# Performance work log

Measured on AMD Instinct MI355X. Metric: run time of the kernel, lower is better.

## Reference

```python
import jax, jax.numpy as jnp
import numpy as np

H = 1024      # hidden_size
E = 8         # num_experts
I = 4 * H     # intermediate_size
B, S = 2, 2048


def setup_inputs() -> dict:
    key = jax.random.key(0)
    ks = jax.random.split(key, 7)
    s_h = 1.0 / np.sqrt(H)
    s_i = 1.0 / np.sqrt(I)
    return {
        "x": jax.random.normal(ks[0], (B, S, H), dtype=jnp.float32),
        "gate_w": jax.random.uniform(ks[1], (H, E), jnp.float32, -s_h, s_h),
        "gate_b": jax.random.uniform(ks[2], (E,), jnp.float32, -s_h, s_h),
        "W1": jax.random.uniform(ks[3], (E, H, I), jnp.float32, -s_h, s_h),
        "b1": jax.random.uniform(ks[4], (E, I), jnp.float32, -s_h, s_h),
        "W2": jax.random.uniform(ks[5], (E, I, H), jnp.float32, -s_i, s_i),
        "b2": jax.random.uniform(ks[6], (E, H), jnp.float32, -s_i, s_i),
    }


def reference(x, gate_w, gate_b, W1, b1, W2, b2):
    b, s, h = x.shape
    flat = x.reshape(-1, h)                      # [T, H]
    T = flat.shape[0]
    e = gate_b.shape[0]

    # Router: softmax -> top-2 -> renormalize
    logits = flat @ gate_w + gate_b              # [T, E]
    probs = jax.nn.softmax(logits, axis=-1)
    top_w, top_idx = jax.lax.top_k(probs, 2)     # [T, 2]
    top_w = top_w / (top_w.sum(axis=-1, keepdims=True) + 1e-6)

    # Dense per-token gate weight matrix [T, E] (0 except top-2 slots)
    gate_full = jnp.zeros((T, e), flat.dtype).at[
        jnp.arange(T)[:, None], top_idx
    ].add(top_w)

    # All experts on all tokens (dense, math-equivalent combine via gate_full)
    hmid = jax.nn.gelu(jnp.einsum('th,ehi->eti', flat, W1) + b1[:, None, :],
                       approximate=True)         # [E, T, I]
    y = jnp.einsum('eti,eih->eth', hmid, W2) + b2[:, None, :]  # [E, T, H]
    out = jnp.einsum('te,eth->th', gate_full, y)  # weighted combine
    return out.reshape(b, s, h)
```

## Files before the change

### kernel.cpp

```cpp
#include <hip/hip_runtime.h>
#include <hip/hip_bf16.h>
#include <math.h>

#define H_DIM 1024
#define E_NUM 8
#define I_DIM 4096
#define T_NUM 4096
#define CAP   8192

typedef __attribute__((ext_vector_type(8))) short bf16x8;
typedef __attribute__((ext_vector_type(4))) float f32x4;

typedef const __attribute__((address_space(1))) void* gptr_t;
typedef __attribute__((address_space(3))) void* lptr_t;

__device__ inline unsigned short f2bf(float f) {
  union { __hip_bfloat16 h; unsigned short u; } cv;
  cv.h = __float2bfloat16(f);
  return cv.u;
}

__global__ void router_kernel(const float* __restrict__ x,
                              const float* __restrict__ gw,
                              const float* __restrict__ gb,
                              int* __restrict__ cnt,
                              int* __restrict__ list,
                              float* __restrict__ tokw) {
  const int t = blockIdx.x;
  const int l = threadIdx.x;
  const float* xr = x + (size_t)t * H_DIM;
  float acc[E_NUM];
#pragma unroll
  for (int e = 0; e < E_NUM; ++e) acc[e] = 0.f;
#pragma unroll
  for (int j = 0; j < H_DIM / 64; ++j) {
    const int h = l + j * 64;
    const float xv = xr[h];
    const float4* g = (const float4*)(gw + (size_t)h * E_NUM);
    const float4 g0 = g[0], g1 = g[1];
    acc[0] += xv * g0.x; acc[1] += xv * g0.y; acc[2] += xv * g0.z; acc[3] += xv * g0.w;
    acc[4] += xv * g1.x; acc[5] += xv * g1.y; acc[6] += xv * g1.z; acc[7] += xv * g1.w;
  }
#pragma unroll
  for (int off = 32; off > 0; off >>= 1) {
#pragma unroll
    for (int e = 0; e < E_NUM; ++e) acc[e] += __shfl_down(acc[e], off, 64);
  }
  if (l == 0) {
    float lg[E_NUM], mx = -1e30f;
#pragma unroll
    for (int e = 0; e < E_NUM; ++e) { lg[e] = acc[e] + gb[e]; mx = fmaxf(mx, lg[e]); }
    float p[E_NUM], s = 0.f;
#pragma unroll
    for (int e = 0; e < E_NUM; ++e) { p[e] = expf(lg[e] - mx); s += p[e]; }
    const float inv = 1.f / s;
#pragma unroll
    for (int e = 0; e < E_NUM; ++e) p[e] *= inv;
    int i0 = 0;
#pragma unroll
    for (int e = 1; e < E_NUM; ++e) if (p[e] > p[i0]) i0 = e;
    int i1 = (i0 == 0) ? 1 : 0;
#pragma unroll
    for (int e = 0; e < E_NUM; ++e) if (e != i0 && p[e] > p[i1]) i1 = e;
    const float denom = p[i0] + p[i1] + 1e-6f;
    const float w0 = p[i0] / denom, w1 = p[i1] / denom;
    int pos = atomicAdd(&cnt[i0], 1);
    list[i0 * CAP + pos] = t * 2;
    tokw[t * 2] = w0;
    pos = atomicAdd(&cnt[i1], 1);
    list[i1 * CAP + pos] = t * 2 + 1;
    tokw[t * 2 + 1] = w1;
  }
}

__global__ void scan_kernel(const int* __restrict__ cnt, int* __restrict__ base) {
  if (threadIdx.x == 0 && blockIdx.x == 0) {
    int b = 0;
    for (int e = 0; e < E_NUM; ++e) { base[e] = b; b += cnt[e]; }
  }
}

__launch_bounds__(256)
__global__ void cvt_x_kernel(const float* __restrict__ x, unsigned short* __restrict__ xb) {
  const size_t i = ((size_t)blockIdx.x * 256 + threadIdx.x) * 8;
  const float4 v0 = *(const float4*)(x + i);
  const float4 v1 = *(const float4*)(x + i + 4);
  unsigned short t[8];
  t[0] = f2bf(v0.x); t[1] = f2bf(v0.y); t[2] = f2bf(v0.z); t[3] = f2bf(v0.w);
  t[4] = f2bf(v1.x); t[5] = f2bf(v1.y); t[6] = f2bf(v1.z); t[7] = f2bf(v1.w);
  *(f32x4*)(xb + i) = *(const f32x4*)t;
}

__launch_bounds__(256)
__global__ void transpose_cvt_kernel(const float* __restrict__ src,
                                     unsigned short* __restrict__ dst,
                                     int R, int C) {
  const int e = blockIdx.z;
  const int r0 = blockIdx.y * 32;
  const int c0 = blockIdx.x * 128;
  const float* s = src + (size_t)e * R * C;
  unsigned short* d = dst + (size_t)e * R * C;
  __shared__ unsigned short Lt[32 * 130];
  const int tid = threadIdx.x;
#pragma unroll
  for (int m = 0; m < 4; ++m) {
    const int li = tid + m * 256;
    const int r = li >> 5;
    const int cg = (li & 31) * 4;
    const float4 v = *(const float4*)(s + (size_t)(r0 + r) * C + c0 + cg);
    Lt[r * 130 + cg + 0] = f2bf(v.x);
    Lt[r * 130 + cg + 1] = f2bf(v.y);
    Lt[r * 130 + cg + 2] = f2bf(v.z);
    Lt[r * 130 + cg + 3] = f2bf(v.w);
  }
  __syncthreads();
#pragma unroll
  for (int m = 0; m < 2; ++m) {
    const int li = tid + m * 256;
    const int col = li >> 2;
    const int rg = (li & 3) * 8;
    unsigned short tmp[8];
#pragma unroll
    for (int j = 0; j < 8; ++j) tmp[j] = Lt[(rg + j) * 130 + col];
    *(f32x4*)(d + (size_t)(c0 + col) * R + r0 + rg) = *(const f32x4*)tmp;
  }
}

__launch_bounds__(256)
__global__ void gemm1_pre_kernel(const unsigned short* __restrict__ xb,
                                 const unsigned short* __restrict__ W1t,
                                 const float* __restrict__ b1,
                                 const int* __restrict__ cnt,
                                 const int* __restrict__ base,
                                 const int* __restrict__ list,
                                 unsigned short* __restrict__ hmid) {
  const int e = blockIdx.z;
  const int c = cnt[e];
  const int m0 = blockIdx.y * 128;
  if (m0 >= c) return;
  const int n0 = blockIdx.x * 128;

  __shared__ int toks[128];
  __shared__ __align__(16) unsigned short As[128 * 32];
  __shared__ __align__(16) unsigned short Bs[128 * 32];

  const int tid = threadIdx.x;
  if (tid < 128) {
    int idx = m0 + tid; if (idx >= c) idx = c - 1;
    toks[tid] = list[e * CAP + idx] >> 1;
  }
  __syncthreads();

  const int lane = tid & 63;
  const int wave = tid >> 6;
  const int wm = (wave >> 1) * 64;
  const int wn = (wave & 1) * 64;
  const int l16 = lane & 15;
  const int quad = lane >> 4;

  const int rA0 = tid >> 2;
  const int rA1 = rA0 + 64;
  const int kg0 = (tid & 3) * 8;
  const unsigned short* W1e = W1t + (size_t)e * H_DIM * I_DIM;

  const unsigned short* aSrc0 = xb + (size_t)toks[rA0] * H_DIM + kg0;
  const unsigned short* aSrc1 = xb + (size_t)toks[rA1] * H_DIM + kg0;
  const unsigned short* bSrc0 = W1e + (size_t)(n0 + rA0) * H_DIM + kg0;
  const unsigned short* bSrc1 = W1e + (size_t)(n0 + rA1) * H_DIM + kg0;
  char* aDst0 = (char*)As + wave * 1024;
  char* aDst1 = (char*)As + 4096 + wave * 1024;
  char* bDst0 = (char*)Bs + wave * 1024;
  char* bDst1 = (char*)Bs + 4096 + wave * 1024;

  f32x4 acc[16];
#pragma unroll
  for (int i = 0; i < 16; ++i) acc[i] = (f32x4){0.f, 0.f, 0.f, 0.f};

  for (int k0 = 0; k0 < H_DIM; k0 += 32) {
    __builtin_amdgcn_global_load_lds((gptr_t)(aSrc0 + k0), (lptr_t)aDst0, 16, 0, 0);
    __builtin_amdgcn_global_load_lds((gptr_t)(aSrc1 + k0), (lptr_t)aDst1, 16, 0, 0);
    __builtin_amdgcn_global_load_lds((gptr_t)(bSrc0 + k0), (lptr_t)bDst0, 16, 0, 0);
    __builtin_amdgcn_global_load_lds((gptr_t)(bSrc1 + k0), (lptr_t)bDst1, 16, 0, 0);
    __syncthreads();
    bf16x8 a[4], b[4];
#pragma unroll
    for (int mf = 0; mf < 4; ++mf)
      a[mf] = *(const bf16x8*)&As[(wm + mf * 16 + l16) * 32 + quad * 8];
#pragma unroll
    for (int nf = 0; nf < 4; ++nf)
      b[nf] = *(const bf16x8*)&Bs[(wn + nf * 16 + l16) * 32 + quad * 8];
#pragma unroll
    for (int mf = 0; mf < 4; ++mf)
#pragma unroll
      for (int nf = 0; nf < 4; ++nf)
        acc[mf * 4 + nf] = __builtin_amdgcn_mfma_f32_16x16x32_bf16(
            a[mf], b[nf], acc[mf * 4 + nf], 0, 0, 0);
    __syncthreads();
  }

  const int hb = base[e];
#pragma unroll
  for (int mf = 0; mf < 4; ++mf) {
#pragma unroll
    for (int reg = 0; reg < 4; ++reg) {
      const int row = wm + mf * 16 + quad * 4 + reg;
      const int gr = m0 + row;
      if (gr < c) {
#pragma unroll
        for (int nf = 0; nf < 4; ++nf) {
          const int col = n0 + wn + nf * 16 + l16;
          const float v = acc[mf * 4 + nf][reg] + b1[e * I_DIM + col];
          const float u = v + 0.044715f * v * v * v;
          const float g = v / (1.f + __expf(-1.5957691216057308f * u));
          hmid[(size_t)(hb + gr) * I_DIM + col] = f2bf(g);
        }
      }
    }
  }
}

__launch_bounds__(256)
__global__ void gemm2_pre_kernel(const unsigned short* __restrict__ hmid,
                                 const unsigned short* __restrict__ W2t,
                                 const float* __restrict__ b2,
                                 const int* __restrict__ cnt,
                                 const int* __restrict__ base,
                                 const int* __restrict__ list,
                                 const float* __restrict__ tokw,
                                 float* __restrict__ out) {
  const int e = blockIdx.z;
  const int c = cnt[e];
  const int m0 = blockIdx.y * 128;
  if (m0 >= c) return;
  const int n0 = blockIdx.x * 128;

  __shared__ int ents[128];
  __shared__ int arow[128];
  __shared__ __align__(16) unsigned short As[128 * 32];
  __shared__ __align__(16) unsigned short Bs[128 * 32];

  const int tid = threadIdx.x;
  const int hb = base[e];
  if (tid < 128) {
    int idx = m0 + tid; if (idx >= c) idx = c - 1;
    ents[tid] = list[e * CAP + idx];
    arow[tid] = hb + idx;
  }
  __syncthreads();

  const int lane = tid & 63;
  const int wave = tid >> 6;
  const int wm = (wave >> 1) * 64;
  const int wn = (wave & 1) * 64;
  const int l16 = lane & 15;
  const int quad = lane >> 4;

  const int rA0 = tid >> 2;
  const int rA1 = rA0 + 64;
  const int kg0 = (tid & 3) * 8;
  const unsigned short* W2e = W2t + (size_t)e * I_DIM * H_DIM;

  const unsigned short* aSrc0 = hmid + (size_t)arow[rA0] * I_DIM + kg0;
  const unsigned short* aSrc1 = hmid + (size_t)arow[rA1] * I_DIM + kg0;
  const unsigned short* bSrc0 = W2e + (size_t)(n0 + rA0) * I_DIM + kg0;
  const unsigned short* bSrc1 = W2e + (size_t)(n0 + rA1) * I_DIM + kg0;
  char* aDst0 = (char*)As + wave * 1024;
  char* aDst1 = (char*)As + 4096 + wave * 1024;
  char* bDst0 = (char*)Bs + wave * 1024;
  char* bDst1 = (char*)Bs + 4096 + wave * 1024;

  f32x4 acc[16];
#pragma unroll
  for (int i = 0; i < 16; ++i) acc[i] = (f32x4){0.f, 0.f, 0.f, 0.f};

  for (int k0 = 0; k0 < I_DIM; k0 += 32) {
    __builtin_amdgcn_global_load_lds((gptr_t)(aSrc0 + k0), (lptr_t)aDst0, 16, 0, 0);
    __builtin_amdgcn_global_load_lds((gptr_t)(aSrc1 + k0), (lptr_t)aDst1, 16, 0, 0);
    __builtin_amdgcn_global_load_lds((gptr_t)(bSrc0 + k0), (lptr_t)bDst0, 16, 0, 0);
    __builtin_amdgcn_global_load_lds((gptr_t)(bSrc1 + k0), (lptr_t)bDst1, 16, 0, 0);
    __syncthreads();
    bf16x8 a[4], b[4];
#pragma unroll
    for (int mf = 0; mf < 4; ++mf)
      a[mf] = *(const bf16x8*)&As[(wm + mf * 16 + l16) * 32 + quad * 8];
#pragma unroll
    for (int nf = 0; nf < 4; ++nf)
      b[nf] = *(const bf16x8*)&Bs[(wn + nf * 16 + l16) * 32 + quad * 8];
#pragma unroll
    for (int mf = 0; mf < 4; ++mf)
#pragma unroll
      for (int nf = 0; nf < 4; ++nf)
        acc[mf * 4 + nf] = __builtin_amdgcn_mfma_f32_16x16x32_bf16(
            a[mf], b[nf], acc[mf * 4 + nf], 0, 0, 0);
    __syncthreads();
  }

#pragma unroll
  for (int mf = 0; mf < 4; ++mf) {
#pragma unroll
    for (int reg = 0; reg < 4; ++reg) {
      const int row = wm + mf * 16 + quad * 4 + reg;
      const int gr = m0 + row;
      if (gr < c) {
        const int ent = ents[row];
        const int t = ent >> 1;
        const float wgt = tokw[ent];
#pragma unroll
        for (int nf = 0; nf < 4; ++nf) {
          const int col = n0 + wn + nf * 16 + l16;
          const float v = acc[mf * 4 + nf][reg] + b2[e * H_DIM + col];
          atomicAdd(&out[(size_t)t * H_DIM + col], wgt * v);
        }
      }
    }
  }
}

__launch_bounds__(256)
__global__ void gemm1_fb_kernel(const float* __restrict__ x,
                                const float* __restrict__ W1,
                                const float* __restrict__ b1,
                                const int* __restrict__ cnt,
                                const int* __restrict__ base,
                                const int* __restrict__ list,
                                unsigned short* __restrict__ hmid) {
  const int e = blockIdx.z;
  const int c = cnt[e];
  const int m0 = blockIdx.y * 128;
  if (m0 >= c) return;
  const int n0 = blockIdx.x * 128;
  __shared__ int toks[128];
  __shared__ __align__(16) unsigned short As[128 * 40];
  __shared__ __align__(16) unsigned short Bs[128 * 40];
  const int tid = threadIdx.x;
  if (tid < 128) {
    int idx = m0 + tid; if (idx >= c) idx = c - 1;
    toks[tid] = list[e * CAP + idx] >> 1;
  }
  __syncthreads();
  const int lane = tid & 63, wave = tid >> 6;
  const int wm = (wave >> 1) * 64, wn = (wave & 1) * 64;
  const int l16 = lane & 15, quad = lane >> 4;
  f32x4 acc[16];
#pragma unroll
  for (int i = 0; i < 16; ++i) acc[i] = (f32x4){0.f, 0.f, 0.f, 0.f};
  const float* W1e = W1 + (size_t)e * H_DIM * I_DIM;
  for (int kt = 0; kt < H_DIM / 32; ++kt) {
    const int k0 = kt * 32;
#pragma unroll
    for (int i = 0; i < 2; ++i) {
      const int idx = tid + i * 256;
      const int row = idx >> 2, g = idx & 3;
      const float* src = x + (size_t)toks[row] * H_DIM + k0 + g * 8;
      const float4 v0 = *(const float4*)(src);
      const float4 v1 = *(const float4*)(src + 4);
      unsigned short tmp[8];
      tmp[0] = f2bf(v0.x); tmp[1] = f2bf(v0.y); tmp[2] = f2bf(v0.z); tmp[3] = f2bf(v0.w);
      tmp[4] = f2bf(v1.x); tmp[5] = f2bf(v1.y); tmp[6] = f2bf(v1.z); tmp[7] = f2bf(v1.w);
      *(f32x4*)&As[row * 40 + g * 8] = *(const f32x4*)tmp;
    }
#pragma unroll
    for (int i = 0; i < 2; ++i) {
      const int idx = tid + i * 256;
      const int n = idx & 127, g = idx >> 7;
      const float* src = W1e + (size_t)(k0 + g * 8) * I_DIM + n0 + n;
      unsigned short tmp[8];
#pragma unroll
      for (int kk = 0; kk < 8; ++kk) tmp[kk] = f2bf(src[(size_t)kk * I_DIM]);
      *(f32x4*)&Bs[n * 40 + g * 8] = *(const f32x4*)tmp;
    }
    __syncthreads();
    bf16x8 a[4], b[4];
#pragma unroll
    for (int mf = 0; mf < 4; ++mf)
      a[mf] = *(const bf16x8*)&As[(wm + mf * 16 + l16) * 40 + quad * 8];
#pragma unroll
    for (int nf = 0; nf < 4; ++nf)
      b[nf] = *(const bf16x8*)&Bs[(wn + nf * 16 + l16) * 40 + quad * 8];
#pragma unroll
    for (int mf = 0; mf < 4; ++mf)
#pragma unroll
      for (int nf = 0; nf < 4; ++nf)
        acc[mf * 4 + nf] = __builtin_amdgcn_mfma_f32_16x16x32_bf16(
            a[mf], b[nf], acc[mf * 4 + nf], 0, 0, 0);
    __syncthreads();
  }
  const int hb = base[e];
#pragma unroll
  for (int mf = 0; mf < 4; ++mf)
#pragma unroll
    for (int reg = 0; reg < 4; ++reg) {
      const int row = wm + mf * 16 + quad * 4 + reg;
      const int gr = m0 + row;
      if (gr < c) {
#pragma unroll
        for (int nf = 0; nf < 4; ++nf) {
          const int col = n0 + wn + nf * 16 + l16;
          const float v = acc[mf * 4 + nf][reg] + b1[e * I_DIM + col];
          const float u = v + 0.044715f * v * v * v;
          const float g = v / (1.f + __expf(-1.5957691216057308f * u));
          hmid[(size_t)(hb + gr) * I_DIM + col] = f2bf(g);
        }
      }
    }
}

__launch_bounds__(256)
__global__ void gemm2_fb_kernel(const unsigned short* __restrict__ hmid,
                                const float* __restrict__ W2,
                                const float* __restrict__ b2,
                                const int* __restrict__ cnt,
                                const int* __restrict__ base,
                                const int* __restrict__ list,
                                const float* __restrict__ tokw,
                                float* __restrict__ out) {
  const int e = blockIdx.z;
  const int c = cnt[e];
  const int m0 = blockIdx.y * 128;
  if (m0 >= c) return;
  const int n0 = blockIdx.x * 128;
  __shared__ int ents[128];
  __shared__ int arow[128];
  __shared__ __align__(16) unsigned short As[128 * 40];
  __shared__ __align__(16) unsigned short Bs[128 * 40];
  const int tid = threadIdx.x;
  const int hb = base[e];
  if (tid < 128) {
    int idx = m0 + tid; if (idx >= c) idx = c - 1;
    ents[tid] = list[e * CAP + idx];
    arow[tid] = hb + idx;
  }
  __syncthreads();
  const int lane = tid & 63, wave = tid >> 6;
  const int wm = (wave >> 1) * 64, wn = (wave & 1) * 64;
  const int l16 = lane & 15, quad = lane >> 4;
  f32x4 acc[16];
#pragma unroll
  for (int i = 0; i < 16; ++i) acc[i] = (f32x4){0.f, 0.f, 0.f, 0.f};
  const float* W2e = W2 + (size_t)e * I_DIM * H_DIM;
  for (int kt = 0; kt < I_DIM / 32; ++kt) {
    const int k0 = kt * 32;
#pragma unroll
    for (int i = 0; i < 2; ++i) {
      const int idx = tid + i * 256;
      const int row = idx >> 2, kg = idx & 3;
      const f32x4 v = *(const f32x4*)(hmid + (size_t)arow[row] * I_DIM + k0 + kg * 8);
      *(f32x4*)&As[row * 40 + kg * 8] = v;
    }
#pragma unroll
    for (int i = 0; i < 2; ++i) {
      const int idx = tid + i * 256;
      const int n = idx & 127, g = idx >> 7;
      const float* src = W2e + (size_t)(k0 + g * 8) * H_DIM + n0 + n;
      unsigned short tmp[8];
#pragma unroll
      for (int kk = 0; kk < 8; ++kk) tmp[kk] = f2bf(src[(size_t)kk * H_DIM]);
      *(f32x4*)&Bs[n * 40 + g * 8] = *(const f32x4*)tmp;
    }
    __syncthreads();
    bf16x8 a[4], b[4];
#pragma unroll
    for (int mf = 0; mf < 4; ++mf)
      a[mf] = *(const bf16x8*)&As[(wm + mf * 16 + l16) * 40 + quad * 8];
#pragma unroll
    for (int nf = 0; nf < 4; ++nf)
      b[nf] = *(const bf16x8*)&Bs[(wn + nf * 16 + l16) * 40 + quad * 8];
#pragma unroll
    for (int mf = 0; mf < 4; ++mf)
#pragma unroll
      for (int nf = 0; nf < 4; ++nf)
        acc[mf * 4 + nf] = __builtin_amdgcn_mfma_f32_16x16x32_bf16(
            a[mf], b[nf], acc[mf * 4 + nf], 0, 0, 0);
    __syncthreads();
  }
#pragma unroll
  for (int mf = 0; mf < 4; ++mf)
#pragma unroll
    for (int reg = 0; reg < 4; ++reg) {
      const int row = wm + mf * 16 + quad * 4 + reg;
      const int gr = m0 + row;
      if (gr < c) {
        const int ent = ents[row];
        const int t = ent >> 1;
        const float wgt = tokw[ent];
#pragma unroll
        for (int nf = 0; nf < 4; ++nf) {
          const int col = n0 + wn + nf * 16 + l16;
          const float v = acc[mf * 4 + nf][reg] + b2[e * H_DIM + col];
          atomicAdd(&out[(size_t)t * H_DIM + col], wgt * v);
        }
      }
    }
}

extern "C" void kernel_launch(void* const* d_in, const int* in_sizes, int n_in,
                              void* d_out, int out_size, void* d_ws, size_t ws_size,
                              hipStream_t stream) {
  (void)in_sizes; (void)n_in;
  const float* x  = (const float*)d_in[0];
  const float* gw = (const float*)d_in[1];
  const float* gb = (const float*)d_in[2];
  const float* W1 = (const float*)d_in[3];
  const float* b1 = (const float*)d_in[4];
  const float* W2 = (const float*)d_in[5];
  const float* b2 = (const float*)d_in[6];
  float* out = (float*)d_out;

  char* w = (char*)d_ws;
  int* cnt    = (int*)w;
  int* base   = (int*)(w + 32);
  int* list   = (int*)(w + 256);
  float* tokw = (float*)(w + 262400);
  unsigned short* hmid = (unsigned short*)(w + 295168);
  unsigned short* W1t  = (unsigned short*)(w + 67404032);
  unsigned short* W2t  = (unsigned short*)(w + 134512896);
  unsigned short* xb   = (unsigned short*)(w + 201621760);
  const size_t NEED = 210010368;

  hipMemsetAsync(cnt, 0, 32, stream);
  hipMemsetAsync(out, 0, (size_t)out_size * sizeof(float), stream);

  router_kernel<<<T_NUM, 64, 0, stream>>>(x, gw, gb, cnt, list, tokw);
  scan_kernel<<<1, 64, 0, stream>>>(cnt, base);

  if (ws_size >= NEED) {
    cvt_x_kernel<<<T_NUM * H_DIM / 2048, 256, 0, stream>>>(x, xb);
    transpose_cvt_kernel<<<dim3(I_DIM / 128, H_DIM / 32, E_NUM), 256, 0, stream>>>(
        W1, W1t, H_DIM, I_DIM);
    transpose_cvt_kernel<<<dim3(H_DIM / 128, I_DIM / 32, E_NUM), 256, 0, stream>>>(
        W2, W2t, I_DIM, H_DIM);
    gemm1_pre_kernel<<<dim3(I_DIM / 128, CAP / 128, E_NUM), 256, 0, stream>>>(
        xb, W1t, b1, cnt, base, list, hmid);
    gemm2_pre_kernel<<<dim3(H_DIM / 128, CAP / 128, E_NUM), 256, 0, stream>>>(
        hmid, W2t, b2, cnt, base, list, tokw, out);
  } else {
    gemm1_fb_kernel<<<dim3(I_DIM / 128, CAP / 128, E_NUM), 256, 0, stream>>>(
        x, W1, b1, cnt, base, list, hmid);
    gemm2_fb_kernel<<<dim3(H_DIM / 128, CAP / 128, E_NUM), 256, 0, stream>>>(
        hmid, W2, b2, cnt, base, list, tokw, out);
  }
}
```

Baseline: 691.0 us.

## Fuse x bf16 convert into router, widen GEMM K-tile with swizzle, split-K gemm2

The router now writes the bf16 copy of x while it reads x, which removes the separate conversion kernel. Both grouped GEMMs use a K-step of 64 with XOR-swizzled LDS layout to reduce bank conflicts and halve the number of barriers per K. gemm2 is split in K into two halves, giving twice as many blocks for better CU occupancy. Both halves already accumulate into the output through atomicAdd, and only one half adds the bias. The cost is double the atomic traffic on the output and a doubled LDS footprint per block.

```diff
diff --git a/kernel.cpp b/kernel.cpp
--- a/kernel.cpp
+++ b/kernel.cpp
@@ -25,7 +25,8 @@
                               const float* __restrict__ gb,
                               int* __restrict__ cnt,
                               int* __restrict__ list,
-                              float* __restrict__ tokw) {
+                              float* __restrict__ tokw,
+                              unsigned short* __restrict__ xb) {
   const int t = blockIdx.x;
   const int l = threadIdx.x;
   const float* xr = x + (size_t)t * H_DIM;
@@ -36,6 +37,7 @@
   for (int j = 0; j < H_DIM / 64; ++j) {
     const int h = l + j * 64;
     const float xv = xr[h];
+    if (xb) xb[(size_t)t * H_DIM + h] = f2bf(xv);
     const float4* g = (const float4*)(gw + (size_t)h * E_NUM);
     const float4 g0 = g[0], g1 = g[1];
     acc[0] += xv * g0.x; acc[1] += xv * g0.y; acc[2] += xv * g0.z; acc[3] += xv * g0.w;
@@ -78,17 +80,6 @@
     int b = 0;
     for (int e = 0; e < E_NUM; ++e) { base[e] = b; b += cnt[e]; }
   }
-}
-
-__launch_bounds__(256)
-__global__ void cvt_x_kernel(const float* __restrict__ x, unsigned short* __restrict__ xb) {
-  const size_t i = ((size_t)blockIdx.x * 256 + threadIdx.x) * 8;
-  const float4 v0 = *(const float4*)(x + i);
-  const float4 v1 = *(const float4*)(x + i + 4);
-  unsigned short t[8];
-  t[0] = f2bf(v0.x); t[1] = f2bf(v0.y); t[2] = f2bf(v0.z); t[3] = f2bf(v0.w);
-  t[4] = f2bf(v1.x); t[5] = f2bf(v1.y); t[6] = f2bf(v1.z); t[7] = f2bf(v1.w);
-  *(f32x4*)(xb + i) = *(const f32x4*)t;
 }
 
 __launch_bounds__(256)
@@ -141,8 +132,8 @@
   const int n0 = blockIdx.x * 128;
 
   __shared__ int toks[128];
-  __shared__ __align__(16) unsigned short As[128 * 32];
-  __shared__ __align__(16) unsigned short Bs[128 * 32];
+  __shared__ __align__(16) unsigned short As[128 * 64];
+  __shared__ __align__(16) unsigned short Bs[128 * 64];
 
   const int tid = threadIdx.x;
   if (tid < 128) {
@@ -157,44 +148,52 @@
   const int wn = (wave & 1) * 64;
   const int l16 = lane & 15;
   const int quad = lane >> 4;
-
-  const int rA0 = tid >> 2;
-  const int rA1 = rA0 + 64;
-  const int kg0 = (tid & 3) * 8;
+  const int sw = (quad ^ (l16 & 7)) * 8;
+
   const unsigned short* W1e = W1t + (size_t)e * H_DIM * I_DIM;
 
-  const unsigned short* aSrc0 = xb + (size_t)toks[rA0] * H_DIM + kg0;
-  const unsigned short* aSrc1 = xb + (size_t)toks[rA1] * H_DIM + kg0;
-  const unsigned short* bSrc0 = W1e + (size_t)(n0 + rA0) * H_DIM + kg0;
-  const unsigned short* bSrc1 = W1e + (size_t)(n0 + rA1) * H_DIM + kg0;
-  char* aDst0 = (char*)As + wave * 1024;
-  char* aDst1 = (char*)As + 4096 + wave * 1024;
-  char* bDst0 = (char*)Bs + wave * 1024;
-  char* bDst1 = (char*)Bs + 4096 + wave * 1024;
+  const unsigned short* aSrc[4];
+  unsigned boff[4];
+#pragma unroll
+  for (int r = 0; r < 4; ++r) {
+    const int cch = r * 256 + tid;
+    const int row = cch >> 3;
+    const int g = (cch & 7) ^ (row & 7);
+    aSrc[r] = xb + (size_t)toks[row] * H_DIM + g * 8;
+    boff[r] = (unsigned)(n0 + row) * H_DIM + g * 8;
+  }
+  char* aDstB = (char*)As + wave * 1024;
+  char* bDstB = (char*)Bs + wave * 1024;
 
   f32x4 acc[16];
 #pragma unroll
   for (int i = 0; i < 16; ++i) acc[i] = (f32x4){0.f, 0.f, 0.f, 0.f};
 
-  for (int k0 = 0; k0 < H_DIM; k0 += 32) {
-    __builtin_amdgcn_global_load_lds((gptr_t)(aSrc0 + k0), (lptr_t)aDst0, 16, 0, 0);
-    __builtin_amdgcn_global_load_lds((gptr_t)(aSrc1 + k0), (lptr_t)aDst1, 16, 0, 0);
-    __builtin_amdgcn_global_load_lds((gptr_t)(bSrc0 + k0), (lptr_t)bDst0, 16, 0, 0);
-    __builtin_amdgcn_global_load_lds((gptr_t)(bSrc1 + k0), (lptr_t)bDst1, 16, 0, 0);
-    __syncthreads();
-    bf16x8 a[4], b[4];
-#pragma unroll
-    for (int mf = 0; mf < 4; ++mf)
-      a[mf] = *(const bf16x8*)&As[(wm + mf * 16 + l16) * 32 + quad * 8];
-#pragma unroll
-    for (int nf = 0; nf < 4; ++nf)
-      b[nf] = *(const bf16x8*)&Bs[(wn + nf * 16 + l16) * 32 + quad * 8];
-#pragma unroll
-    for (int mf = 0; mf < 4; ++mf)
+  for (int k0 = 0; k0 < H_DIM; k0 += 64) {
+#pragma unroll
+    for (int r = 0; r < 4; ++r)
+      __builtin_amdgcn_global_load_lds((gptr_t)(aSrc[r] + k0), (lptr_t)(aDstB + r * 4096), 16, 0, 0);
+#pragma unroll
+    for (int r = 0; r < 4; ++r)
+      __builtin_amdgcn_global_load_lds((gptr_t)(W1e + boff[r] + k0), (lptr_t)(bDstB + r * 4096), 16, 0, 0);
+    __syncthreads();
+#pragma unroll
+    for (int kh = 0; kh < 2; ++kh) {
+      const int ko = sw ^ (kh * 32);
+      bf16x8 a[4], b[4];
+#pragma unroll
+      for (int mf = 0; mf < 4; ++mf)
+        a[mf] = *(const bf16x8*)&As[(wm + mf * 16 + l16) * 64 + ko];
 #pragma unroll
       for (int nf = 0; nf < 4; ++nf)
-        acc[mf * 4 + nf] = __builtin_amdgcn_mfma_f32_16x16x32_bf16(
-            a[mf], b[nf], acc[mf * 4 + nf], 0, 0, 0);
+        b[nf] = *(const bf16x8*)&Bs[(wn + nf * 16 + l16) * 64 + ko];
+#pragma unroll
+      for (int mf = 0; mf < 4; ++mf)
+#pragma unroll
+        for (int nf = 0; nf < 4; ++nf)
+          acc[mf * 4 + nf] = __builtin_amdgcn_mfma_f32_16x16x32_bf16(
+              a[mf], b[nf], acc[mf * 4 + nf], 0, 0, 0);
+    }
     __syncthreads();
   }
 
@@ -232,12 +231,15 @@
   const int c = cnt[e];
   const int m0 = blockIdx.y * 128;
   if (m0 >= c) return;
-  const int n0 = blockIdx.x * 128;
+  const int n0 = (blockIdx.x & 7) * 128;
+  const int split = blockIdx.x >> 3;
+  const int kbeg = split * (I_DIM / 2);
+  const int kend = kbeg + I_DIM / 2;
 
   __shared__ int ents[128];
   __shared__ int arow[128];
-  __shared__ __align__(16) unsigned short As[128 * 32];
-  __shared__ __align__(16) unsigned short Bs[128 * 32];
+  __shared__ __align__(16) unsigned short As[128 * 64];
+  __shared__ __align__(16) unsigned short Bs[128 * 64];
 
   const int tid = threadIdx.x;
   const int hb = base[e];
@@ -254,44 +256,52 @@
   const int wn = (wave & 1) * 64;
   const int l16 = lane & 15;
   const int quad = lane >> 4;
-
-  const int rA0 = tid >> 2;
-  const int rA1 = rA0 + 64;
-  const int kg0 = (tid & 3) * 8;
+  const int sw = (quad ^ (l16 & 7)) * 8;
+
   const unsigned short* W2e = W2t + (size_t)e * I_DIM * H_DIM;
 
-  const unsigned short* aSrc0 = hmid + (size_t)arow[rA0] * I_DIM + kg0;
-  const unsigned short* aSrc1 = hmid + (size_t)arow[rA1] * I_DIM + kg0;
-  const unsigned short* bSrc0 = W2e + (size_t)(n0 + rA0) * I_DIM + kg0;
-  const unsigned short* bSrc1 = W2e + (size_t)(n0 + rA1) * I_DIM + kg0;
-  char* aDst0 = (char*)As + wave * 1024;
-  char* aDst1 = (char*)As + 4096 + wave * 1024;
-  char* bDst0 = (char*)Bs + wave * 1024;
-  char* bDst1 = (char*)Bs + 4096 + wave * 1024;
+  const unsigned short* aSrc[4];
+  unsigned boff[4];
+#pragma unroll
+  for (int r = 0; r < 4; ++r) {
+    const int cch = r * 256 + tid;
+    const int row = cch >> 3;
+    const int g = (cch & 7) ^ (row & 7);
+    aSrc[r] = hmid + (size_t)arow[row] * I_DIM + g * 8;
+    boff[r] = (unsigned)(n0 + row) * I_DIM + g * 8;
+  }
+  char* aDstB = (char*)As + wave * 1024;
+  char* bDstB = (char*)Bs + wave * 1024;
 
   f32x4 acc[16];
 #pragma unroll
   for (int i = 0; i < 16; ++i) acc[i] = (f32x4){0.f, 0.f, 0.f, 0.f};
 
-  for (int k0 = 0; k0 < I_DIM; k0 += 32) {
-    __builtin_amdgcn_global_load_lds((gptr_t)(aSrc0 + k0), (lptr_t)aDst0, 16, 0, 0);
-    __builtin_amdgcn_global_load_lds((gptr_t)(aSrc1 + k0), (lptr_t)aDst1, 16, 0, 0);
-    __builtin_amdgcn_global_load_lds((gptr_t)(bSrc0 + k0), (lptr_t)bDst0, 16, 0, 0);
-    __builtin_amdgcn_global_load_lds((gptr_t)(bSrc1 + k0), (lptr_t)bDst1, 16, 0, 0);
-    __syncthreads();
-    bf16x8 a[4], b[4];
-#pragma unroll
-    for (int mf = 0; mf < 4; ++mf)
-      a[mf] = *(const bf16x8*)&As[(wm + mf * 16 + l16) * 32 + quad * 8];
-#pragma unroll
-    for (int nf = 0; nf < 4; ++nf)
-      b[nf] = *(const bf16x8*)&Bs[(wn + nf * 16 + l16) * 32 + quad * 8];
-#pragma unroll
-    for (int mf = 0; mf < 4; ++mf)
+  for (int k0 = kbeg; k0 < kend; k0 += 64) {
+#pragma unroll
+    for (int r = 0; r < 4; ++r)
+      __builtin_amdgcn_global_load_lds((gptr_t)(aSrc[r] + k0), (lptr_t)(aDstB + r * 4096), 16, 0, 0);
+#pragma unroll
+    for (int r = 0; r < 4; ++r)
+      __builtin_amdgcn_global_load_lds((gptr_t)(W2e + boff[r] + k0), (lptr_t)(bDstB + r * 4096), 16, 0, 0);
+    __syncthreads();
+#pragma unroll
+    for (int kh = 0; kh < 2; ++kh) {
+      const int ko = sw ^ (kh * 32);
+      bf16x8 a[4], b[4];
+#pragma unroll
+      for (int mf = 0; mf < 4; ++mf)
+        a[mf] = *(const bf16x8*)&As[(wm + mf * 16 + l16) * 64 + ko];
 #pragma unroll
       for (int nf = 0; nf < 4; ++nf)
-        acc[mf * 4 + nf] = __builtin_amdgcn_mfma_f32_16x16x32_bf16(
-            a[mf], b[nf], acc[mf * 4 + nf], 0, 0, 0);
+        b[nf] = *(const bf16x8*)&Bs[(wn + nf * 16 + l16) * 64 + ko];
+#pragma unroll
+      for (int mf = 0; mf < 4; ++mf)
+#pragma unroll
+        for (int nf = 0; nf < 4; ++nf)
+          acc[mf * 4 + nf] = __builtin_amdgcn_mfma_f32_16x16x32_bf16(
+              a[mf], b[nf], acc[mf * 4 + nf], 0, 0, 0);
+    }
     __syncthreads();
   }
 
@@ -308,7 +318,8 @@
 #pragma unroll
         for (int nf = 0; nf < 4; ++nf) {
           const int col = n0 + wn + nf * 16 + l16;
-          const float v = acc[mf * 4 + nf][reg] + b2[e * H_DIM + col];
+          float v = acc[mf * 4 + nf][reg];
+          if (split == 0) v += b2[e * H_DIM + col];
           atomicAdd(&out[(size_t)t * H_DIM + col], wgt * v);
         }
       }
@@ -516,22 +527,23 @@
   unsigned short* W2t  = (unsigned short*)(w + 134512896);
   unsigned short* xb   = (unsigned short*)(w + 201621760);
   const size_t NEED = 210010368;
+  const bool pre = (ws_size >= NEED);
 
   hipMemsetAsync(cnt, 0, 32, stream);
   hipMemsetAsync(out, 0, (size_t)out_size * sizeof(float), stream);
 
-  router_kernel<<<T_NUM, 64, 0, stream>>>(x, gw, gb, cnt, list, tokw);
+  router_kernel<<<T_NUM, 64, 0, stream>>>(x, gw, gb, cnt, list, tokw,
+                                          pre ? xb : (unsigned short*)nullptr);
   scan_kernel<<<1, 64, 0, stream>>>(cnt, base);
 
-  if (ws_size >= NEED) {
-    cvt_x_kernel<<<T_NUM * H_DIM / 2048, 256, 0, stream>>>(x, xb);
+  if (pre) {
     transpose_cvt_kernel<<<dim3(I_DIM / 128, H_DIM / 32, E_NUM), 256, 0, stream>>>(
         W1, W1t, H_DIM, I_DIM);
     transpose_cvt_kernel<<<dim3(H_DIM / 128, I_DIM / 32, E_NUM), 256, 0, stream>>>(
         W2, W2t, I_DIM, H_DIM);
     gemm1_pre_kernel<<<dim3(I_DIM / 128, CAP / 128, E_NUM), 256, 0, stream>>>(
         xb, W1t, b1, cnt, base, list, hmid);
-    gemm2_pre_kernel<<<dim3(H_DIM / 128, CAP / 128, E_NUM), 256, 0, stream>>>(
+    gemm2_pre_kernel<<<dim3(2 * (H_DIM / 128), CAP / 128, E_NUM), 256, 0, stream>>>(
         hmid, W2t, b2, cnt, base, list, tokw, out);
   } else {
     gemm1_fb_kernel<<<dim3(I_DIM / 128, CAP / 128, E_NUM), 256, 0, stream>>>(
```

After: 779.5 us. 1.13x slower.
